# Optimization experiments

Hardware: AMD Instinct MI355X
Metric: run time of the kernel (lower is better)

Reference implementation:

```python
import jax, jax.numpy as jnp
import numpy as np

C = 256
EPS = 1e-5


def setup_inputs() -> dict:
    key = jax.random.key(0)
    ks = jax.random.split(key, 11)
    B, L = 4, 4096
    s = 1.0 / np.sqrt(C)
    inp = {
        'x': jax.random.normal(ks[0], (B, C, L), dtype=jnp.float32),
        'gamma': jnp.ones((C,), jnp.float32),
        'beta': jnp.zeros((C,), jnp.float32),
        'wq': jax.random.normal(ks[1], (C, C), jnp.float32) * s,
        'bq': jax.random.normal(ks[2], (C,), jnp.float32) * 0.01,
        'wk': jax.random.normal(ks[3], (C, C), jnp.float32) * s,
        'bk': jax.random.normal(ks[4], (C,), jnp.float32) * 0.01,
        'wv': jax.random.normal(ks[5], (C, C), jnp.float32) * s,
        'bv': jax.random.normal(ks[6], (C,), jnp.float32) * 0.01,
        'wp': jax.random.normal(ks[7], (C, C), jnp.float32) * s,
        'bp': jax.random.normal(ks[8], (C,), jnp.float32) * 0.01,
    }
    return inp


def reference(x, gamma, beta, wq, bq, wk, bk, wv, bv, wp, bp):
    # BatchNorm1d (training mode): normalize over batch and length dims
    mean = jnp.mean(x, axis=(0, 2), keepdims=True)          # [1,C,1]
    var = jnp.var(x, axis=(0, 2), keepdims=True)            # biased var, as torch BN
    h = (x - mean) * jax.lax.rsqrt(var + EPS)
    h = h * gamma[None, :, None] + beta[None, :, None]

    # 1x1 convs == channel-mixing matmuls: [C_out,C_in] x [B,C_in,L]
    q = jnp.einsum('oc,bcl->bol', wq, h) + bq[None, :, None]
    k = jnp.einsum('oc,bcl->bol', wk, h) + bk[None, :, None]
    v = jnp.einsum('oc,bcl->bol', wv, h) + bv[None, :, None]

    c = q.shape[1]
    scale = jnp.asarray(int(c) ** (-0.5), q.dtype)
    # w[b,i,j] = sum_c q[b,c,i] k[b,c,j]
    w = jnp.einsum('bci,bcj->bij', q, k) * scale
    w = jax.nn.softmax(w, axis=2)
    # torch: h[b,c,i] = sum_j v[b,c,j] * w[b,i,j]
    h = jnp.einsum('bcj,bij->bci', v, w)

    h = jnp.einsum('oc,bcl->bol', wp, h) + bp[None, :, None]
    return x + h
```

## Files before the change

### kernel.cpp

```cpp
#include <hip/hip_runtime.h>
#include <math.h>

typedef unsigned short u16;
typedef unsigned int u32;
typedef short s16x8 __attribute__((ext_vector_type(8)));
typedef float f32x4 __attribute__((ext_vector_type(4)));
typedef float f32x16 __attribute__((ext_vector_type(16)));

static constexpr int Cc = 256;
static constexpr int Ll = 4096;
static constexpr int Bb = 4;

__device__ __forceinline__ u16 f2b(float f) {
    union { float f; unsigned u; } v; v.f = f;
    unsigned r = v.u + 0x7FFF + ((v.u >> 16) & 1);
    return (u16)(r >> 16);
}
__device__ __forceinline__ float b2f(u16 h) {
    union { unsigned u; float f; } v; v.u = ((unsigned)h) << 16; return v.f;
}

__device__ __forceinline__ void gload_lds16(const u16* g, u16* l) {
    __builtin_amdgcn_global_load_lds(
        (const __attribute__((address_space(1))) u32*)g,
        (__attribute__((address_space(3))) u32*)l, 16, 0, 0);
}

__global__ void k_transpose(const float* __restrict__ x, u16* __restrict__ XT,
                            float* __restrict__ sums) {
    int lt = blockIdx.x, ct = blockIdx.y, b = blockIdx.z, t = threadIdx.x;
    int l0 = lt * 64, c0 = ct * 64;
    __shared__ u16 tile[64][65];
    __shared__ float red[2][4][64];
    int ll = t & 63, cb = t >> 6;
    #pragma unroll
    for (int rep = 0; rep < 16; rep++) {
        int cl = cb * 16 + rep;
        tile[cl][ll] = f2b(x[(size_t)(b * Cc + c0 + cl) * Ll + l0 + ll]);
    }
    __syncthreads();
    int cl2 = t & 63, lb = t >> 6;
    float s = 0.f, s2 = 0.f;
    #pragma unroll
    for (int rep = 0; rep < 16; rep++) {
        int ll2 = lb * 16 + rep;
        u16 hv = tile[cl2][ll2];
        XT[(size_t)(b * Ll + l0 + ll2) * Cc + c0 + cl2] = hv;
        float v = b2f(hv);
        s += v; s2 += v * v;
    }
    red[0][lb][cl2] = s;
    red[1][lb][cl2] = s2;
    __syncthreads();
    if (t < 64) {
        float ss = red[0][0][t] + red[0][1][t] + red[0][2][t] + red[0][3][t];
        float ss2 = red[1][0][t] + red[1][1][t] + red[1][2][t] + red[1][3][t];
        atomicAdd(&sums[c0 + t], ss);
        atomicAdd(&sums[256 + c0 + t], ss2);
    }
}

__global__ void k_fold(const float* __restrict__ wq, const float* __restrict__ bq,
                       const float* __restrict__ wk, const float* __restrict__ bk,
                       const float* __restrict__ wv, const float* __restrict__ bv,
                       const float* __restrict__ wp,
                       const float* __restrict__ gamma, const float* __restrict__ beta,
                       const float* __restrict__ sums,
                       u16* __restrict__ Wqkv, float* __restrict__ biasQKV,
                       u16* __restrict__ Wp16) {
    int m = blockIdx.x, t = threadIdx.x;
    if (m >= 768) {
        int row = m - 768;
        Wp16[row * Cc + t] = f2b(wp[row * Cc + t]);
        return;
    }
    const float inv_n = 1.f / (Bb * Ll);
    float mean = sums[t] * inv_n;
    float var  = sums[256 + t] * inv_n - mean * mean;
    float rstd = rsqrtf(var + 1e-5f);
    float a  = gamma[t] * rstd;
    float cB = beta[t] - mean * a;
    int type = m >> 8, row = m & 255;
    const float* W  = (type == 0) ? wq : (type == 1) ? wk : wv;
    const float* bs = (type == 0) ? bq : (type == 1) ? bk : bv;
    float wval = W[row * Cc + t];
    float s2 = (type == 0) ? 0.09016844005556021f : 1.0f;
    Wqkv[m * Cc + t] = f2b(wval * a * s2);
    __shared__ float rs[256];
    rs[t] = wval * cB;
    __syncthreads();
    for (int off = 128; off > 0; off >>= 1) {
        if (t < off) rs[t] += rs[t + off];
        __syncthreads();
    }
    if (t == 0) biasQKV[m] = (bs[row] + rs[0]) * s2;
}

__launch_bounds__(256, 2)
__global__ void k_qkv(const u16* __restrict__ XT, const u16* __restrict__ Wqkv,
                      const float* __restrict__ biasQKV,
                      u16* __restrict__ QT, u16* __restrict__ KT, u16* __restrict__ V) {
    int ly = blockIdx.x, b = blockIdx.y;
    int t = threadIdx.x, w = t >> 6, lane = t & 63;
    int l16 = lane & 15, quad = lane >> 4;
    int l0 = ly * 64;
    __shared__ u16 Xs[64][264];
    {
        int row = t >> 2, chunk = t & 3;
        const u16* src = XT + (size_t)(b * Ll + l0 + row) * Cc + chunk * 64;
        u16* dst = &Xs[row][chunk * 64];
        #pragma unroll
        for (int u = 0; u < 8; u++)
            *(uint4*)(dst + u * 8) = *(const uint4*)(src + u * 8);
    }
    __syncthreads();
    for (int ox = 0; ox < 12; ox++) {
        int o0 = ox * 64;
        s16x8 af[8];
        {
            const u16* wrow = Wqkv + (size_t)(o0 + w * 16 + l16) * Cc + quad * 8;
            #pragma unroll
            for (int ks = 0; ks < 8; ks++) af[ks] = *(const s16x8*)(wrow + ks * 32);
        }
        f32x4 acc[4];
        #pragma unroll
        for (int ns = 0; ns < 4; ns++)
            #pragma unroll
            for (int r = 0; r < 4; r++) acc[ns][r] = 0.f;
        #pragma unroll
        for (int ks = 0; ks < 8; ks++) {
            #pragma unroll
            for (int ns = 0; ns < 4; ns++) {
                s16x8 bf = *(const s16x8*)(&Xs[ns * 16 + l16][ks * 32 + quad * 8]);
                acc[ns] = __builtin_amdgcn_mfma_f32_16x16x32_bf16(af[ks], bf, acc[ns], 0, 0, 0);
            }
        }
        int obase = o0 + w * 16 + quad * 4;
        float bias[4];
        #pragma unroll
        for (int r = 0; r < 4; r++) bias[r] = biasQKV[obase + r];
        #pragma unroll
        for (int ns = 0; ns < 4; ns++) {
            int l = l0 + ns * 16 + l16;
            if (ox < 8) {
                u16* dstbase = (ox < 4) ? QT : KT;
                int oo = obase - ((ox < 4) ? 0 : 256);
                ushort4 pk;
                pk.x = f2b(acc[ns][0] + bias[0]);
                pk.y = f2b(acc[ns][1] + bias[1]);
                pk.z = f2b(acc[ns][2] + bias[2]);
                pk.w = f2b(acc[ns][3] + bias[3]);
                *(ushort4*)(dstbase + (size_t)(b * Ll + l) * Cc + oo) = pk;
            } else {
                #pragma unroll
                for (int r = 0; r < 4; r++) {
                    int o = obase + r - 512;
                    V[(size_t)(b * Cc + o) * Ll + l] = f2b(acc[ns][r] + bias[r]);
                }
            }
        }
    }
}

__launch_bounds__(512, 2)
__global__ void k_attn(const u16* __restrict__ QT, const u16* __restrict__ KT,
                       const u16* __restrict__ V, u16* __restrict__ Opart,
                       float* __restrict__ Lpart) {
    int id = blockIdx.x;
    int xcd = id & 7, local = id >> 3;
    int b = xcd >> 1;
    int u = local * 2 + (xcd & 1);
    int itile = u >> 1;
    int jh = u & 1;
    int t = threadIdx.x, w = t >> 6, lane = t & 63;
    int rh = w & 3, ch = w >> 2;
    int l31 = lane & 31, hi = lane >> 5;

    __shared__ u16 Ka[16384];
    __shared__ u16 Vbuf[16384];
    __shared__ u16 Pss[128 * 72];
    __shared__ float Lred[4][2][32];

    s16x8 qf[16];
    {
        const u16* qbase = QT + (size_t)(b * Ll + itile * 128 + rh * 32 + l31) * Cc + hi * 8;
        #pragma unroll
        for (int ks = 0; ks < 16; ks++) qf[ks] = *(const s16x8*)(qbase + ks * 16);
    }

    const u16* kptr[4];
    const u16* vptr[4];
    #pragma unroll
    for (int R = 0; R < 4; R++) {
        int g = R * 8 + w;
        int gch = g >> 4, gks = g & 15;
        kptr[R] = KT + (size_t)(b * Ll + jh * 2048 + gch * 32 + l31) * Cc + gks * 16 + hi * 8;
        int gct = g >> 2, gkj = g & 3;
        vptr[R] = V + (size_t)(b * Cc + gct * 32 + l31) * Ll + jh * 2048 + gkj * 16 + hi * 8;
    }

    #pragma unroll
    for (int R = 0; R < 4; R++) {
        gload_lds16(kptr[R], &Ka[(size_t)((R * 8 + w) * 64) * 8]);
        kptr[R] += 64 * Cc;
    }
    #pragma unroll
    for (int R = 0; R < 4; R++) {
        gload_lds16(vptr[R], &Vbuf[(size_t)((R * 8 + w) * 64) * 8]);
        vptr[R] += 64;
    }

    f32x16 of16[4];
    #pragma unroll
    for (int ct = 0; ct < 4; ct++)
        #pragma unroll
        for (int r = 0; r < 16; r++) of16[ct][r] = 0.f;
    f32x16 lsr;
    #pragma unroll
    for (int r = 0; r < 16; r++) lsr[r] = 0.f;

    __syncthreads();

    for (int it = 0; it < 32; it++) {
        f32x16 s0, s1;
        #pragma unroll
        for (int r = 0; r < 16; r++) { s0[r] = 0.f; s1[r] = 0.f; }
        #pragma unroll
        for (int ks = 0; ks < 16; ks += 2) {
            s16x8 bf0 = *(const s16x8*)(&Ka[(size_t)((ch * 16 + ks) * 64 + lane) * 8]);
            s16x8 bf1 = *(const s16x8*)(&Ka[(size_t)((ch * 16 + ks + 1) * 64 + lane) * 8]);
            s0 = __builtin_amdgcn_mfma_f32_32x32x16_bf16(qf[ks], bf0, s0, 0, 0, 0);
            s1 = __builtin_amdgcn_mfma_f32_32x32x16_bf16(qf[ks + 1], bf1, s1, 0, 0, 0);
        }
        #pragma unroll
        for (int reg = 0; reg < 16; reg++) {
            float p = __builtin_amdgcn_exp2f(s0[reg] + s1[reg]);
            lsr[reg] += p;
            int row_local = (reg & 3) + 8 * (reg >> 2) + 4 * hi;
            Pss[(rh * 32 + row_local) * 72 + ch * 32 + l31] = f2b(p);
        }
        __syncthreads();
        if (it < 31) {
            #pragma unroll
            for (int R = 0; R < 4; R++) {
                gload_lds16(kptr[R], &Ka[(size_t)((R * 8 + w) * 64) * 8]);
                kptr[R] += 64 * Cc;
            }
        }
        #pragma unroll
        for (int ksj = 0; ksj < 4; ksj++) {
            s16x8 pa = *(const s16x8*)(&Pss[(rh * 32 + l31) * 72 + ksj * 16 + hi * 8]);
            #pragma unroll
            for (int ct = 0; ct < 4; ct++) {
                s16x8 bf = *(const s16x8*)(&Vbuf[(size_t)(((ch * 4 + ct) * 4 + ksj) * 64 + lane) * 8]);
                of16[ct] = __builtin_amdgcn_mfma_f32_32x32x16_bf16(pa, bf, of16[ct], 0, 0, 0);
            }
        }
        __syncthreads();
        if (it < 31) {
            #pragma unroll
            for (int R = 0; R < 4; R++) {
                gload_lds16(vptr[R], &Vbuf[(size_t)((R * 8 + w) * 64) * 8]);
                vptr[R] += 64;
            }
        }
    }
    #pragma unroll
    for (int reg = 0; reg < 16; reg++) {
        float v = lsr[reg];
        #pragma unroll
        for (int off = 16; off > 0; off >>= 1) v += __shfl_xor(v, off);
        int row_local = (reg & 3) + 8 * (reg >> 2) + 4 * hi;
        if (l31 == 0) Lred[rh][ch][row_local] = v;
    }
    __syncthreads();
    int mi0 = (jh * 4 + b) * Ll + itile * 128 + rh * 32;
    if (ch == 0 && lane < 32)
        Lpart[mi0 + lane] = Lred[rh][0][lane] + Lred[rh][1][lane];
    #pragma unroll
    for (int ct = 0; ct < 4; ct++) {
        #pragma unroll
        for (int reg = 0; reg < 16; reg++) {
            int row_local = (reg & 3) + 8 * (reg >> 2) + 4 * hi;
            Opart[(size_t)(mi0 + row_local) * 256 + ch * 128 + ct * 32 + l31] =
                f2b(of16[ct][reg]);
        }
    }
}

__global__ void k_merge(const u16* __restrict__ Opart, const float* __restrict__ Lpart,
                        u16* __restrict__ OT) {
    int id = blockIdx.x, t = threadIdx.x;
    int b = id >> 6, itile = id & 63;
    int row = t >> 2, seg = t & 3;
    size_t i0 = ((size_t)(0 + b) * 64 + itile) * 64 + row;
    size_t i1 = ((size_t)(4 + b) * 64 + itile) * 64 + row;
    float inv = 1.f / (Lpart[i0] + Lpart[i1]);
    const u16* p0 = Opart + i0 * 256 + seg * 64;
    const u16* p1 = Opart + i1 * 256 + seg * 64;
    u16* dst = OT + (size_t)(b * Ll + itile * 64 + row) * Cc + seg * 64;
    #pragma unroll
    for (int k = 0; k < 8; k++) {
        ushort4 a0 = *(const ushort4*)(p0 + k * 8 + 0);
        ushort4 b0 = *(const ushort4*)(p0 + k * 8 + 4);
        ushort4 a1 = *(const ushort4*)(p1 + k * 8 + 0);
        ushort4 b1 = *(const ushort4*)(p1 + k * 8 + 4);
        ushort4 oA, oB;
        oA.x = f2b((b2f(a0.x) + b2f(a1.x)) * inv);
        oA.y = f2b((b2f(a0.y) + b2f(a1.y)) * inv);
        oA.z = f2b((b2f(a0.z) + b2f(a1.z)) * inv);
        oA.w = f2b((b2f(a0.w) + b2f(a1.w)) * inv);
        oB.x = f2b((b2f(b0.x) + b2f(b1.x)) * inv);
        oB.y = f2b((b2f(b0.y) + b2f(b1.y)) * inv);
        oB.z = f2b((b2f(b0.z) + b2f(b1.z)) * inv);
        oB.w = f2b((b2f(b0.w) + b2f(b1.w)) * inv);
        *(ushort4*)(dst + k * 8 + 0) = oA;
        *(ushort4*)(dst + k * 8 + 4) = oB;
    }
}

__launch_bounds__(256, 2)
__global__ void k_proj(const u16* __restrict__ OT, const u16* __restrict__ Opart,
                       const float* __restrict__ Lpart, int fused,
                       const u16* __restrict__ Wp16,
                       const float* __restrict__ bp, const float* __restrict__ x,
                       float* __restrict__ out) {
    int ly = blockIdx.x, b = blockIdx.y;
    int t = threadIdx.x, w = t >> 6, lane = t & 63;
    int l16 = lane & 15, quad = lane >> 4;
    int l0 = ly * 64;
    __shared__ u16 Os[64][264];
    {
        int row = t >> 2, chunk = t & 3;
        u16* dst = &Os[row][chunk * 64];
        if (fused) {
            size_t i0 = ((size_t)(0 + b) * Ll + l0 + row);
            size_t i1 = ((size_t)(4 + b) * Ll + l0 + row);
            float inv = 1.f / (Lpart[i0] + Lpart[i1]);
            const u16* p0 = Opart + i0 * 256 + chunk * 64;
            const u16* p1 = Opart + i1 * 256 + chunk * 64;
            #pragma unroll
            for (int k = 0; k < 8; k++) {
                ushort4 a0 = *(const ushort4*)(p0 + k * 8 + 0);
                ushort4 b0 = *(const ushort4*)(p0 + k * 8 + 4);
                ushort4 a1 = *(const ushort4*)(p1 + k * 8 + 0);
                ushort4 b1 = *(const ushort4*)(p1 + k * 8 + 4);
                ushort4 oA, oB;
                oA.x = f2b((b2f(a0.x) + b2f(a1.x)) * inv);
                oA.y = f2b((b2f(a0.y) + b2f(a1.y)) * inv);
                oA.z = f2b((b2f(a0.z) + b2f(a1.z)) * inv);
                oA.w = f2b((b2f(a0.w) + b2f(a1.w)) * inv);
                oB.x = f2b((b2f(b0.x) + b2f(b1.x)) * inv);
                oB.y = f2b((b2f(b0.y) + b2f(b1.y)) * inv);
                oB.z = f2b((b2f(b0.z) + b2f(b1.z)) * inv);
                oB.w = f2b((b2f(b0.w) + b2f(b1.w)) * inv);
                *(ushort4*)(dst + k * 8 + 0) = oA;
                *(ushort4*)(dst + k * 8 + 4) = oB;
            }
        } else {
            const u16* src = OT + (size_t)(b * Ll + l0 + row) * Cc + chunk * 64;
            #pragma unroll
            for (int u = 0; u < 8; u++)
                *(uint4*)(dst + u * 8) = *(const uint4*)(src + u * 8);
        }
    }
    __syncthreads();
    for (int ox = 0; ox < 4; ox++) {
        int o0 = ox * 64;
        s16x8 af[8];
        {
            const u16* wrow = Wp16 + (size_t)(o0 + w * 16 + l16) * Cc + quad * 8;
            #pragma unroll
            for (int ks = 0; ks < 8; ks++) af[ks] = *(const s16x8*)(wrow + ks * 32);
        }
        f32x4 acc[4];
        #pragma unroll
        for (int ns = 0; ns < 4; ns++)
            #pragma unroll
            for (int r = 0; r < 4; r++) acc[ns][r] = 0.f;
        #pragma unroll
        for (int ks = 0; ks < 8; ks++) {
            #pragma unroll
            for (int ns = 0; ns < 4; ns++) {
                s16x8 bf = *(const s16x8*)(&Os[ns * 16 + l16][ks * 32 + quad * 8]);
                acc[ns] = __builtin_amdgcn_mfma_f32_16x16x32_bf16(af[ks], bf, acc[ns], 0, 0, 0);
            }
        }
        int ob = o0 + w * 16 + quad * 4;
        float bias[4];
        #pragma unroll
        for (int r = 0; r < 4; r++) bias[r] = bp[ob + r];
        #pragma unroll
        for (int ns = 0; ns < 4; ns++) {
            #pragma unroll
            for (int r = 0; r < 4; r++) {
                int o = ob + r;
                int l = l0 + ns * 16 + l16;
                size_t idx = (size_t)(b * Cc + o) * Ll + l;
                out[idx] = x[idx] + bias[r] + acc[ns][r];
            }
        }
    }
}

extern "C" void kernel_launch(void* const* d_in, const int* in_sizes, int n_in,
                              void* d_out, int out_size, void* d_ws, size_t ws_size,
                              hipStream_t stream) {
    const float* x     = (const float*)d_in[0];
    const float* gamma = (const float*)d_in[1];
    const float* beta  = (const float*)d_in[2];
    const float* wq    = (const float*)d_in[3];
    const float* bq    = (const float*)d_in[4];
    const float* wk    = (const float*)d_in[5];
    const float* bk    = (const float*)d_in[6];
    const float* wv    = (const float*)d_in[7];
    const float* bv    = (const float*)d_in[8];
    const float* wp    = (const float*)d_in[9];
    const float* bp    = (const float*)d_in[10];
    float* out = (float*)d_out;
    char* ws = (char*)d_ws;

    float* sums    = (float*)(ws + 0);
    float* biasQKV = (float*)(ws + 2048);
    u16*   Wqkv    = (u16*)(ws + 8192);
    u16*   Wp16    = (u16*)(ws + 401408);
    u16*   XT      = (u16*)(ws + 532480);
    u16*   QT      = (u16*)(ws + 8921088);
    u16*   KT      = (u16*)(ws + 17309696);
    u16*   V       = (u16*)(ws + 25698304);
    u16*   OT      = XT;

    const size_t opart_off = 34086912;
    const size_t lpart_off = opart_off + 16777216;
    const size_t needed    = lpart_off + 131072;
    int fused = (ws_size >= needed) ? 1 : 0;
    u16*   Opart = fused ? (u16*)(ws + opart_off) : (u16*)d_out;
    float* Lpart = (float*)(ws + (fused ? lpart_off : opart_off));

    hipMemsetAsync(sums, 0, 2048, stream);
    k_transpose<<<dim3(64, 4, 4), 256, 0, stream>>>(x, XT, sums);
    k_fold<<<1024, 256, 0, stream>>>(wq, bq, wk, bk, wv, bv, wp, gamma, beta,
                                     sums, Wqkv, biasQKV, Wp16);
    k_qkv<<<dim3(64, 4), 256, 0, stream>>>(XT, Wqkv, biasQKV, QT, KT, V);
    k_attn<<<256, 512, 0, stream>>>(QT, KT, V, Opart, Lpart);
    if (!fused)
        k_merge<<<256, 256, 0, stream>>>(Opart, Lpart, OT);
    k_proj<<<dim3(64, 4), 256, 0, stream>>>(OT, Opart, Lpart, fused,
                                            Wp16, bp, x, out);
}
```

Measured before the change: 227.4 us.

## Double-buffer K/V tiles in attention kernel with fine-grained vmcnt waits

Turns the single K and V LDS buffers into two-stage ping-pong buffers, so the tile for iteration it+2 is fetched while iteration it computes. __syncthreads is replaced by explicit s_waitcnt vmcnt/lgkmcnt counts and raw s_barrier calls, and s_setprio is raised around the MFMA loops. The goal is to hide global-to-LDS load latency behind the QK and PV matrix work. In exchange LDS use roughly doubles, which may limit the 2-blocks-per-CU occupancy, and correctness now depends on the hand-counted vmcnt values.

```diff
diff --git a/kernel.cpp b/kernel.cpp
--- a/kernel.cpp
+++ b/kernel.cpp
@@ -176,8 +176,8 @@
     int rh = w & 3, ch = w >> 2;
     int l31 = lane & 31, hi = lane >> 5;
 
-    __shared__ u16 Ka[16384];
-    __shared__ u16 Vbuf[16384];
+    __shared__ u16 Ka[2][16384];
+    __shared__ u16 Vbuf[2][16384];
     __shared__ u16 Pss[128 * 72];
     __shared__ float Lred[4][2][32];
 
@@ -201,12 +201,22 @@
 
     #pragma unroll
     for (int R = 0; R < 4; R++) {
-        gload_lds16(kptr[R], &Ka[(size_t)((R * 8 + w) * 64) * 8]);
+        gload_lds16(kptr[R], &Ka[0][(size_t)(R * 8 + w) * 512]);
         kptr[R] += 64 * Cc;
     }
     #pragma unroll
     for (int R = 0; R < 4; R++) {
-        gload_lds16(vptr[R], &Vbuf[(size_t)((R * 8 + w) * 64) * 8]);
+        gload_lds16(vptr[R], &Vbuf[0][(size_t)(R * 8 + w) * 512]);
+        vptr[R] += 64;
+    }
+    #pragma unroll
+    for (int R = 0; R < 4; R++) {
+        gload_lds16(kptr[R], &Ka[1][(size_t)(R * 8 + w) * 512]);
+        kptr[R] += 64 * Cc;
+    }
+    #pragma unroll
+    for (int R = 0; R < 4; R++) {
+        gload_lds16(vptr[R], &Vbuf[1][(size_t)(R * 8 + w) * 512]);
         vptr[R] += 64;
     }
 
@@ -219,19 +229,25 @@
     #pragma unroll
     for (int r = 0; r < 16; r++) lsr[r] = 0.f;
 
-    __syncthreads();
-
     for (int it = 0; it < 32; it++) {
+        const u16* KaC = Ka[it & 1];
+        const u16* VbC = Vbuf[it & 1];
+        if (it < 31) asm volatile("s_waitcnt vmcnt(12)" ::: "memory");
+        else         asm volatile("s_waitcnt vmcnt(4)"  ::: "memory");
+        __builtin_amdgcn_s_barrier();
+
         f32x16 s0, s1;
         #pragma unroll
         for (int r = 0; r < 16; r++) { s0[r] = 0.f; s1[r] = 0.f; }
+        __builtin_amdgcn_s_setprio(1);
         #pragma unroll
         for (int ks = 0; ks < 16; ks += 2) {
-            s16x8 bf0 = *(const s16x8*)(&Ka[(size_t)((ch * 16 + ks) * 64 + lane) * 8]);
-            s16x8 bf1 = *(const s16x8*)(&Ka[(size_t)((ch * 16 + ks + 1) * 64 + lane) * 8]);
+            s16x8 bf0 = *(const s16x8*)(&KaC[(size_t)((ch * 16 + ks) * 64 + lane) * 8]);
+            s16x8 bf1 = *(const s16x8*)(&KaC[(size_t)((ch * 16 + ks + 1) * 64 + lane) * 8]);
             s0 = __builtin_amdgcn_mfma_f32_32x32x16_bf16(qf[ks], bf0, s0, 0, 0, 0);
             s1 = __builtin_amdgcn_mfma_f32_32x32x16_bf16(qf[ks + 1], bf1, s1, 0, 0, 0);
         }
+        __builtin_amdgcn_s_setprio(0);
         #pragma unroll
         for (int reg = 0; reg < 16; reg++) {
             float p = __builtin_amdgcn_exp2f(s0[reg] + s1[reg]);
@@ -239,28 +255,37 @@
             int row_local = (reg & 3) + 8 * (reg >> 2) + 4 * hi;
             Pss[(rh * 32 + row_local) * 72 + ch * 32 + l31] = f2b(p);
         }
-        __syncthreads();
-        if (it < 31) {
+        asm volatile("s_waitcnt lgkmcnt(0)" ::: "memory");
+        __builtin_amdgcn_s_barrier();
+        if (it < 30) {
             #pragma unroll
             for (int R = 0; R < 4; R++) {
-                gload_lds16(kptr[R], &Ka[(size_t)((R * 8 + w) * 64) * 8]);
+                gload_lds16(kptr[R], &Ka[it & 1][(size_t)(R * 8 + w) * 512]);
                 kptr[R] += 64 * Cc;
             }
         }
+        if (it < 30)      asm volatile("s_waitcnt vmcnt(12)" ::: "memory");
+        else if (it == 30) asm volatile("s_waitcnt vmcnt(8)" ::: "memory");
+        else              asm volatile("s_waitcnt vmcnt(0)" ::: "memory");
+        __builtin_amdgcn_s_barrier();
+
+        __builtin_amdgcn_s_setprio(1);
         #pragma unroll
         for (int ksj = 0; ksj < 4; ksj++) {
             s16x8 pa = *(const s16x8*)(&Pss[(rh * 32 + l31) * 72 + ksj * 16 + hi * 8]);
             #pragma unroll
             for (int ct = 0; ct < 4; ct++) {
-                s16x8 bf = *(const s16x8*)(&Vbuf[(size_t)(((ch * 4 + ct) * 4 + ksj) * 64 + lane) * 8]);
+                s16x8 bf = *(const s16x8*)(&VbC[(size_t)(((ch * 4 + ct) * 4 + ksj) * 64 + lane) * 8]);
                 of16[ct] = __builtin_amdgcn_mfma_f32_32x32x16_bf16(pa, bf, of16[ct], 0, 0, 0);
             }
         }
-        __syncthreads();
-        if (it < 31) {
+        __builtin_amdgcn_s_setprio(0);
+        asm volatile("s_waitcnt lgkmcnt(0)" ::: "memory");
+        __builtin_amdgcn_s_barrier();
+        if (it < 30) {
             #pragma unroll
             for (int R = 0; R < 4; R++) {
-                gload_lds16(vptr[R], &Vbuf[(size_t)((R * 8 + w) * 64) * 8]);
+                gload_lds16(vptr[R], &Vbuf[it & 1][(size_t)(R * 8 + w) * 512]);
                 vptr[R] += 64;
             }
         }
```

New measurement: 228.4 us. No clear change (+0.4%).

## Restructure attention kernel with double-buffered K/V and register-resident P

Applied to the files above, without the earlier changes.

Rewrites the attention inner loop so K and V tiles are double-buffered in a single 128KB LDS buffer with explicit vmcnt waits, letting the global loads for the next tile overlap compute. The score MFMA swaps operands, so the P tile comes out in a layout that v_cvt_pk_bf16 plus permlane32_swap can turn directly into A-operands. This removes the round trip of P through LDS and one barrier per iteration. Work is now split across key subsets: each wave covers all 256 output channels for its key half, and a final LDS reduction combines the two halves. It also adds s_setprio around the MFMA blocks. The cost is higher LDS use, which likely limits occupancy to one block per CU, more accumulator registers (8 f32x16), and fragile hand-written waitcnt logic.

```diff
diff --git a/kernel.cpp b/kernel.cpp
--- a/kernel.cpp
+++ b/kernel.cpp
@@ -24,6 +24,12 @@
     __builtin_amdgcn_global_load_lds(
         (const __attribute__((address_space(1))) u32*)g,
         (__attribute__((address_space(3))) u32*)l, 16, 0, 0);
+}
+
+__device__ __forceinline__ u32 cvtpk(float lo, float hi) {
+    u32 r;
+    asm volatile("v_cvt_pk_bf16_f32 %0, %1, %2" : "=v"(r) : "v"(lo), "v"(hi));
+    return r;
 }
 
 __global__ void k_transpose(const float* __restrict__ x, u16* __restrict__ XT,
@@ -173,118 +179,145 @@
     int itile = u >> 1;
     int jh = u & 1;
     int t = threadIdx.x, w = t >> 6, lane = t & 63;
-    int rh = w & 3, ch = w >> 2;
+    int iw = w & 3, jsub = w >> 2;
     int l31 = lane & 31, hi = lane >> 5;
 
-    __shared__ u16 Ka[16384];
-    __shared__ u16 Vbuf[16384];
-    __shared__ u16 Pss[128 * 72];
-    __shared__ float Lred[4][2][32];
+    __shared__ u16 lds_buf[65536];
+    __shared__ float Lred[2][4][32];
 
     s16x8 qf[16];
     {
-        const u16* qbase = QT + (size_t)(b * Ll + itile * 128 + rh * 32 + l31) * Cc + hi * 8;
+        const u16* qbase = QT + (size_t)(b * Ll + itile * 128 + iw * 32 + l31) * Cc + hi * 8;
         #pragma unroll
         for (int ks = 0; ks < 16; ks++) qf[ks] = *(const s16x8*)(qbase + ks * 16);
     }
 
-    const u16* kptr[4];
-    const u16* vptr[4];
+    const u16* kcur = KT + (size_t)(b * Ll + jh * 2048 + l31) * Cc + hi * 8;
+    const u16* vcur = V + (size_t)(b * Cc + l31) * Ll + jh * 2048 + hi * 8;
+    int kwo = w * 16;
+    size_t vwo = (size_t)((w >> 2) * 32) * Ll + (w & 3) * 16;
+    int ldw = w * 512;
+
+#define STAGE_K(c) { u16* kd = lds_buf + (c) * 16384 + ldw;  \
+    gload_lds16(kcur + kwo,        kd);          \
+    gload_lds16(kcur + kwo + 128,  kd + 4096);   \
+    gload_lds16(kcur + kwo + 8192, kd + 8192);   \
+    gload_lds16(kcur + kwo + 8320, kd + 12288);  \
+    kcur += 64 * Cc; }
+#define STAGE_V(c) { u16* vd = lds_buf + 32768 + (c) * 16384 + ldw;  \
+    gload_lds16(vcur + vwo,          vd);          \
+    gload_lds16(vcur + vwo + 262144, vd + 4096);   \
+    gload_lds16(vcur + vwo + 524288, vd + 8192);   \
+    gload_lds16(vcur + vwo + 786432, vd + 12288);  \
+    vcur += 64; }
+
+    STAGE_K(0); STAGE_V(0); STAGE_K(1); STAGE_V(1);
+
+    f32x16 of[8];
     #pragma unroll
-    for (int R = 0; R < 4; R++) {
-        int g = R * 8 + w;
-        int gch = g >> 4, gks = g & 15;
-        kptr[R] = KT + (size_t)(b * Ll + jh * 2048 + gch * 32 + l31) * Cc + gks * 16 + hi * 8;
-        int gct = g >> 2, gkj = g & 3;
-        vptr[R] = V + (size_t)(b * Cc + gct * 32 + l31) * Ll + jh * 2048 + gkj * 16 + hi * 8;
-    }
-
-    #pragma unroll
-    for (int R = 0; R < 4; R++) {
-        gload_lds16(kptr[R], &Ka[(size_t)((R * 8 + w) * 64) * 8]);
-        kptr[R] += 64 * Cc;
-    }
-    #pragma unroll
-    for (int R = 0; R < 4; R++) {
-        gload_lds16(vptr[R], &Vbuf[(size_t)((R * 8 + w) * 64) * 8]);
-        vptr[R] += 64;
-    }
-
-    f32x16 of16[4];
-    #pragma unroll
-    for (int ct = 0; ct < 4; ct++)
-        #pragma unroll
-        for (int r = 0; r < 16; r++) of16[ct][r] = 0.f;
-    f32x16 lsr;
-    #pragma unroll
-    for (int r = 0; r < 16; r++) lsr[r] = 0.f;
-
-    __syncthreads();
+    for (int ct = 0; ct < 8; ct++)
+        #pragma unroll
+        for (int r = 0; r < 16; r++) of[ct][r] = 0.f;
+    float lsum = 0.f;
+
+    asm volatile("s_waitcnt vmcnt(12)" ::: "memory");
+    __builtin_amdgcn_s_barrier();
+
+    int aoff = jsub * 8192 + lane * 8;
+    int boff = jsub * 1024 + lane * 8;
 
     for (int it = 0; it < 32; it++) {
+        const u16* KaC = lds_buf + (it & 1) * 16384;
+        const u16* VbC = lds_buf + 32768 + (it & 1) * 16384;
+
         f32x16 s0, s1;
         #pragma unroll
         for (int r = 0; r < 16; r++) { s0[r] = 0.f; s1[r] = 0.f; }
+        __builtin_amdgcn_s_setprio(1);
         #pragma unroll
         for (int ks = 0; ks < 16; ks += 2) {
-            s16x8 bf0 = *(const s16x8*)(&Ka[(size_t)((ch * 16 + ks) * 64 + lane) * 8]);
-            s16x8 bf1 = *(const s16x8*)(&Ka[(size_t)((ch * 16 + ks + 1) * 64 + lane) * 8]);
-            s0 = __builtin_amdgcn_mfma_f32_32x32x16_bf16(qf[ks], bf0, s0, 0, 0, 0);
-            s1 = __builtin_amdgcn_mfma_f32_32x32x16_bf16(qf[ks + 1], bf1, s1, 0, 0, 0);
-        }
-        #pragma unroll
-        for (int reg = 0; reg < 16; reg++) {
-            float p = __builtin_amdgcn_exp2f(s0[reg] + s1[reg]);
-            lsr[reg] += p;
-            int row_local = (reg & 3) + 8 * (reg >> 2) + 4 * hi;
-            Pss[(rh * 32 + row_local) * 72 + ch * 32 + l31] = f2b(p);
-        }
-        __syncthreads();
+            s16x8 kf0 = *(const s16x8*)(KaC + aoff + ks * 512);
+            s16x8 kf1 = *(const s16x8*)(KaC + aoff + ks * 512 + 512);
+            s0 = __builtin_amdgcn_mfma_f32_32x32x16_bf16(kf0, qf[ks], s0, 0, 0, 0);
+            s1 = __builtin_amdgcn_mfma_f32_32x32x16_bf16(kf1, qf[ks + 1], s1, 0, 0, 0);
+        }
+        __builtin_amdgcn_s_setprio(0);
+
+        float p[16];
+        #pragma unroll
+        for (int r = 0; r < 16; r++) {
+            p[r] = __builtin_amdgcn_exp2f(s0[r] + s1[r]);
+            lsum += p[r];
+        }
+        u32 paw[2][4];
+        #pragma unroll
+        for (int js = 0; js < 2; js++) {
+            int o = js * 8;
+            u32 a0 = cvtpk(p[o + 0], p[o + 1]);
+            u32 b0 = cvtpk(p[o + 4], p[o + 5]);
+            u32 a1 = cvtpk(p[o + 2], p[o + 3]);
+            u32 b1 = cvtpk(p[o + 6], p[o + 7]);
+            asm volatile("v_permlane32_swap_b32 %0, %1" : "+v"(a0), "+v"(b0));
+            asm volatile("v_permlane32_swap_b32 %0, %1" : "+v"(a1), "+v"(b1));
+            paw[js][0] = a0; paw[js][1] = a1; paw[js][2] = b0; paw[js][3] = b1;
+        }
+
+        asm volatile("s_waitcnt lgkmcnt(0)" ::: "memory");
+        if (it < 31) asm volatile("s_waitcnt vmcnt(8)" ::: "memory");
+        else         asm volatile("s_waitcnt vmcnt(0)" ::: "memory");
+        __builtin_amdgcn_s_barrier();
+        if (it < 30) STAGE_K(it & 1);
+
+        __builtin_amdgcn_s_setprio(1);
+        #pragma unroll
+        for (int js = 0; js < 2; js++) {
+            union { u32 u[4]; s16x8 v; } pa;
+            pa.u[0] = paw[js][0]; pa.u[1] = paw[js][1];
+            pa.u[2] = paw[js][2]; pa.u[3] = paw[js][3];
+            #pragma unroll
+            for (int ct = 0; ct < 8; ct++) {
+                s16x8 bf = *(const s16x8*)(VbC + ct * 2048 + boff + js * 512);
+                of[ct] = __builtin_amdgcn_mfma_f32_32x32x16_bf16(pa.v, bf, of[ct], 0, 0, 0);
+            }
+        }
+        __builtin_amdgcn_s_setprio(0);
+
         if (it < 31) {
-            #pragma unroll
-            for (int R = 0; R < 4; R++) {
-                gload_lds16(kptr[R], &Ka[(size_t)((R * 8 + w) * 64) * 8]);
-                kptr[R] += 64 * Cc;
-            }
-        }
-        #pragma unroll
-        for (int ksj = 0; ksj < 4; ksj++) {
-            s16x8 pa = *(const s16x8*)(&Pss[(rh * 32 + l31) * 72 + ksj * 16 + hi * 8]);
-            #pragma unroll
-            for (int ct = 0; ct < 4; ct++) {
-                s16x8 bf = *(const s16x8*)(&Vbuf[(size_t)(((ch * 4 + ct) * 4 + ksj) * 64 + lane) * 8]);
-                of16[ct] = __builtin_amdgcn_mfma_f32_32x32x16_bf16(pa, bf, of16[ct], 0, 0, 0);
-            }
-        }
-        __syncthreads();
-        if (it < 31) {
-            #pragma unroll
-            for (int R = 0; R < 4; R++) {
-                gload_lds16(vptr[R], &Vbuf[(size_t)((R * 8 + w) * 64) * 8]);
-                vptr[R] += 64;
-            }
-        }
-    }
-    #pragma unroll
-    for (int reg = 0; reg < 16; reg++) {
-        float v = lsr[reg];
-        #pragma unroll
-        for (int off = 16; off > 0; off >>= 1) v += __shfl_xor(v, off);
-        int row_local = (reg & 3) + 8 * (reg >> 2) + 4 * hi;
-        if (l31 == 0) Lred[rh][ch][row_local] = v;
-    }
-    __syncthreads();
-    int mi0 = (jh * 4 + b) * Ll + itile * 128 + rh * 32;
-    if (ch == 0 && lane < 32)
-        Lpart[mi0 + lane] = Lred[rh][0][lane] + Lred[rh][1][lane];
-    #pragma unroll
-    for (int ct = 0; ct < 4; ct++) {
-        #pragma unroll
-        for (int reg = 0; reg < 16; reg++) {
-            int row_local = (reg & 3) + 8 * (reg >> 2) + 4 * hi;
-            Opart[(size_t)(mi0 + row_local) * 256 + ch * 128 + ct * 32 + l31] =
-                f2b(of16[ct][reg]);
-        }
+            asm volatile("s_waitcnt lgkmcnt(0)" ::: "memory");
+            if (it < 30) asm volatile("s_waitcnt vmcnt(8)" ::: "memory");
+            else         asm volatile("s_waitcnt vmcnt(4)" ::: "memory");
+            __builtin_amdgcn_s_barrier();
+            if (it < 30) STAGE_V(it & 1);
+        }
+    }
+#undef STAGE_K
+#undef STAGE_V
+
+    lsum += __shfl_xor(lsum, 32);
+    if (lane < 32) Lred[jsub][iw][l31] = lsum;
+    __syncthreads();
+    int mi0 = (jh * 4 + b) * Ll + itile * 128;
+    if (jsub == 0 && lane < 32)
+        Lpart[mi0 + iw * 32 + l31] = Lred[0][iw][l31] + Lred[1][iw][l31];
+
+    float* Om = (float*)lds_buf;
+    if (jsub == 1) {
+        #pragma unroll
+        for (int ct = 0; ct < 8; ct++)
+            #pragma unroll
+            for (int r = 0; r < 16; r++)
+                Om[((iw * 8 + ct) * 16 + r) * 64 + lane] = of[ct][r];
+    }
+    __syncthreads();
+    if (jsub == 0) {
+        #pragma unroll
+        for (int ct = 0; ct < 8; ct++)
+            #pragma unroll
+            for (int r = 0; r < 16; r++) {
+                float val = of[ct][r] + Om[((iw * 8 + ct) * 16 + r) * 64 + lane];
+                int rl = (r & 3) + 8 * (r >> 2) + 4 * hi;
+                Opart[(size_t)(mi0 + iw * 32 + rl) * 256 + ct * 32 + l31] = f2b(val);
+            }
     }
 }
 
@@ -437,7 +470,7 @@
     u16*   Opart = fused ? (u16*)(ws + opart_off) : (u16*)d_out;
     float* Lpart = (float*)(ws + (fused ? lpart_off : opart_off));
 
-    hipMemsetAsync(sums, 0, 2048, stream);
+    (void)hipMemsetAsync(sums, 0, 2048, stream);
     k_transpose<<<dim3(64, 4, 4), 256, 0, stream>>>(x, XT, sums);
     k_fold<<<1024, 256, 0, stream>>>(wq, bq, wk, bk, wv, bv, wp, gamma, beta,
                                      sums, Wqkv, biasQKV, Wp16);
```

New measurement: 224.4 us. No clear change (-1.3%).
